# Kernel tuning notes

Measured on AMD Instinct MI355X. Metric: run time of the kernel, lower is better.

The kernel has to match this reference:

```python
import jax, jax.numpy as jnp
import numpy as np

EPS = 1e-8
SEARCH = 21  # search_window_size


def _window_stack(x, S):
    """x: [B,C,Hp,Wp] (already padded). Returns [B,C,H,W,S*S] matching
    torch unfold(2,S,1).unfold(3,S,1).reshape(...,-1) ordering (h-offset major)."""
    B, C, Hp, Wp = x.shape
    H, W = Hp - S + 1, Wp - S + 1
    patches = jax.lax.conv_general_dilated_patches(
        x, filter_shape=(S, S), window_strides=(1, 1), padding='VALID',
        dimension_numbers=('NCHW', 'OIHW', 'NCHW'))  # [B, C*S*S, H, W], (C, u, v) major->minor
    patches = patches.reshape(B, C, S * S, H, W)
    return jnp.transpose(patches, (0, 1, 3, 4, 2))  # [B,C,H,W,S*S]


def setup_inputs() -> dict:
    key = jax.random.key(0)
    k1, k2 = jax.random.split(key)
    rgb = jax.random.uniform(k1, (1, 3, 256, 256), dtype=jnp.float32)  # must be in [0,1]
    h = jnp.array([0.1], dtype=jnp.float32)  # learned NLM bandwidth parameter
    return {"rgb": rgb, "h": h}


def reference(rgb, h):
    S = SEARCH
    pad = (S - 1) // 2
    # luminance (clip only affects y, not the rgb values being averaged)
    rgb_c = jnp.clip(rgb, 0.0, 1.0)
    y = 0.299 * rgb_c[:, :1] + 0.587 * rgb_c[:, 1:2] + 0.114 * rgb_c[:, 2:]  # [B,1,H,W]

    pw = ((0, 0), (0, 0), (pad, pad), (pad, pad))
    rgb_ws = _window_stack(jnp.pad(rgb, pw, mode='reflect'), S)  # [B,3,H,W,S^2]
    y_ws = _window_stack(jnp.pad(y, pw, mode='reflect'), S)      # [B,1,H,W,S^2]

    dis = (y[..., None] - y_ws) ** 2                              # [B,1,H,W,S^2]
    dis_pad = jnp.pad(dis, ((0, 0), (0, 0), (pad, pad), (pad, pad), (0, 0)), mode='reflect')
    # sum of squared diffs over an SxS spatial window per offset (matches unfold+sum)
    dis = jax.lax.reduce_window(dis_pad, 0.0, jax.lax.add,
                                (1, 1, S, S, 1), (1, 1, 1, 1, 1), 'VALID')  # [B,1,H,W,S^2]

    distances = jnp.sqrt(jax.nn.relu(dis))
    weights = jnp.exp(-distances / (jax.nn.relu(h) + EPS))        # [B,1,H,W,S^2]
    denoised = (weights * rgb_ws).sum(-1) / weights.sum(-1)       # [B,3,H,W]
    return jnp.clip(denoised, 0.0, 1.0)
```

## Files before the change

kernel.cpp:

```cpp
#include <hip/hip_runtime.h>
#include <math.h>


#define IMG 256
#define NPIX (IMG * IMG)
#define TILE 32
#define GR 52
#define YD 72
#define YSTR 78
#define HST 54
#define NOFF 441
#define NGB 12

typedef __attribute__((ext_vector_type(4))) _Float16 half4;
typedef __attribute__((ext_vector_type(2))) _Float16 half2_t;

#if __has_builtin(__builtin_amdgcn_fdot2)
#define FDOT2(a, b, c) __builtin_amdgcn_fdot2((a), (b), (c), false)
#else
#define FDOT2(a, b, c) ((c) + (float)(a).x * (float)(b).x + (float)(a).y * (float)(b).y)
#endif

__device__ __forceinline__ int refl(int t) {
    t = t < 0 ? -t : t;
    return t > 255 ? 510 - t : t;
}

template <bool DIRECT>
__global__ __launch_bounds__(256, 3)
void nlm_main(const float* __restrict__ rgb, const float* __restrict__ hptr,
              float4* __restrict__ partials)
{
    __shared__ __align__(16) _Float16 Yreg[YD][YSTR];
    __shared__ __align__(16) _Float16 Creg4[GR][GR][4];
    __shared__ __align__(16) _Float16 hsT[4][TILE][HST];
    __shared__ unsigned char cjTab[21][GR];

    const int tid = threadIdx.x;
    const int tj = ((int)blockIdx.x & 7) * TILE;
    const int ti = ((int)blockIdx.x >> 3) * TILE;

    const int Ybi = min(max(ti - 20, 0), IMG - YD);
    const int Ybj = min(max(tj - 20, 0), IMG - YD);
    const bool interior = (ti >= 20) && (ti + 51 <= 255) && (tj >= 20) && (tj + 51 <= 255);

    for (int idx = tid; idx < YD * YD; idx += 256) {
        int a = idx / YD, b = idx - a * YD;
        int g = (Ybi + a) * IMG + (Ybj + b);
        float r  = fminf(fmaxf(rgb[g], 0.f), 1.f);
        float gg = fminf(fmaxf(rgb[NPIX + g], 0.f), 1.f);
        float bb = fminf(fmaxf(rgb[2 * NPIX + g], 0.f), 1.f);
        Yreg[a][b] = (_Float16)(0.299f * r + 0.587f * gg + 0.114f * bb);
    }
    for (int idx = tid; idx < GR * GR; idx += 256) {
        int t = idx / GR, b = idx - t * GR;
        int g = refl(ti - 10 + t) * IMG + refl(tj - 10 + b);
        half4 c;
        c.x = (_Float16)rgb[g];
        c.y = (_Float16)rgb[NPIX + g];
        c.z = (_Float16)rgb[2 * NPIX + g];
        c.w = (_Float16)0.f;
        *(half4*)&Creg4[t][b][0] = c;
    }
    if (!interior) {
        for (int idx = tid; idx < 21 * GR; idx += 256) {
            int d = idx / GR, c = idx - d * GR;
            cjTab[d][c] = (unsigned char)(refl(refl(tj - 10 + c) + (d - 10)) - Ybj);
        }
    }
    __syncthreads();

    const int lane = tid & 63;
    const int wv   = tid >> 6;
    const bool hact = lane < GR;

    half2_t y0h[26];
    if (hact) {
        if (interior) {
            const half2_t* q0 = (const half2_t*)&Yreg[lane + 10][10];
            #pragma unroll
            for (int i = 0; i < 26; ++i) y0h[i] = q0[i];
        } else {
            const _Float16* Y0row = &Yreg[refl(ti - 10 + lane) - Ybi][0];
            const unsigned char* cj0 = &cjTab[10][0];
            #pragma unroll
            for (int i = 0; i < 26; ++i) {
                half2_t v;
                v.x = Y0row[cj0[2 * i]];
                v.y = Y0row[cj0[2 * i + 1]];
                y0h[i] = v;
            }
        }
    }

    const float hv = fmaxf(hptr[0], 0.f);
    const float negI = -1.0f / (hv + 1e-8f);

    const int pb  = lane & 31;
    const int s16 = (lane >> 5) << 4;

    float aR[16], aG[16], aB[16], aW[16];
    #pragma unroll
    for (int k = 0; k < 16; ++k) { aR[k]=0.f; aG[k]=0.f; aB[k]=0.f; aW[k]=0.f; }

    half2_t one; one.x = (_Float16)1.f; one.y = (_Float16)1.f;

    for (int o = (int)blockIdx.y * 4 + wv; o < NOFF; o += 48) {
        const int oq = o / 21;
        const int du = oq - 10;
        const int dv = o - oq * 21 - 10;

        if (hact) {
            const int t = lane;
            half2_t ff[26];
            if (interior) {
                if ((dv & 1) == 0) {
                    const half2_t* q1 = (const half2_t*)&Yreg[t + 10 + du][10 + dv];
                    #pragma unroll
                    for (int i = 0; i < 26; ++i) {
                        half2_t d2 = y0h[i] - q1[i];
                        ff[i] = d2 * d2;
                    }
                } else {
                    const half2_t* q1 = (const half2_t*)&Yreg[t + 10 + du][10 + dv - 1];
                    half2_t prev = q1[0];
                    #pragma unroll
                    for (int i = 0; i < 26; ++i) {
                        half2_t cur = q1[i + 1];
                        half2_t b; b.x = prev.y; b.y = cur.x;
                        half2_t d2 = y0h[i] - b;
                        ff[i] = d2 * d2;
                        prev = cur;
                    }
                }
            } else {
                const unsigned int* cw = (const unsigned int*)&cjTab[dv + 10][0];
                const _Float16* Y1row = &Yreg[refl(refl(ti - 10 + t) + du) - Ybi][0];
                #pragma unroll
                for (int i = 0; i < 26; ++i) {
                    unsigned int w0 = cw[i >> 1];
                    int sh = (i & 1) * 16;
                    _Float16 a0 = Y1row[(w0 >> sh) & 0xffu];
                    _Float16 a1 = Y1row[(w0 >> (sh + 8)) & 0xffu];
                    half2_t yv; yv.x = a0; yv.y = a1;
                    half2_t d2 = y0h[i] - yv;
                    ff[i] = d2 * d2;
                }
            }
            float s0f = 0.f;
            #pragma unroll
            for (int i = 0; i < 10; ++i) s0f = FDOT2(ff[i], one, s0f);
            s0f += (float)ff[10].x;
            _Float16 s = (_Float16)s0f;
            hsT[wv][0][t] = s;
            #pragma unroll
            for (int k = 1; k < 32; ++k) {
                int ja = 20 + k, jb = k - 1;
                _Float16 fa = (ja & 1) ? ff[ja >> 1].y : ff[ja >> 1].x;
                _Float16 fb = (jb & 1) ? ff[jb >> 1].y : ff[jb >> 1].x;
                s += (_Float16)(fa - fb);
                hsT[wv][k][t] = s;
            }
        }

        {
            const half2_t* col2 = (const half2_t*)&hsT[wv][pb][s16];
            half2_t w2[18];
            #pragma unroll
            for (int i = 0; i < 18; ++i) w2[i] = col2[i];

            float vs = 0.f;
            #pragma unroll
            for (int i = 0; i < 10; ++i) vs = FDOT2(w2[i], one, vs);
            vs += (float)w2[10].x;

            float vss[16];
            vss[0] = vs;
            #pragma unroll
            for (int k = 0; k < 15; ++k) {
                int ja = 21 + k, jb = k;
                _Float16 fa = (ja & 1) ? w2[ja >> 1].y : w2[ja >> 1].x;
                _Float16 fb = (jb & 1) ? w2[jb >> 1].y : w2[jb >> 1].x;
                vss[k + 1] = vss[k] + (float)(_Float16)(fa - fb);
            }

            const int cr = s16 + 10 + du;
            const int cc = pb + 10 + dv;
            #pragma unroll
            for (int k = 0; k < 16; ++k) {
                float dist = sqrtf(fmaxf(vss[k], 0.f));
                float w = __expf(dist * negI);
                half4 c = *(const half4*)&Creg4[cr + k][cc][0];
                aW[k] += w;
                aR[k] += w * (float)c.x;
                aG[k] += w * (float)c.y;
                aB[k] += w * (float)c.z;
            }
        }
    }

    __syncthreads();
    float4* scratch = (float4*)&Creg4[0][0][0];
    #pragma unroll
    for (int w = 0; w < 4; ++w) {
        if (wv == w) {
            #pragma unroll
            for (int k = 0; k < 16; ++k) {
                int px = (s16 + k) * 32 + pb;
                float4 v = make_float4(aR[k], aG[k], aB[k], aW[k]);
                if (w == 0) scratch[px] = v;
                else {
                    float4 a = scratch[px];
                    scratch[px] = make_float4(a.x + v.x, a.y + v.y, a.z + v.z, a.w + v.w);
                }
            }
        }
        __syncthreads();
    }
    for (int i = tid; i < TILE * TILE; i += 256) {
        float4 v = scratch[i];
        int gpix = (ti + (i >> 5)) * IMG + (tj + (i & 31));
        if (DIRECT) {
            partials[(size_t)blockIdx.y * NPIX + gpix] = v;
        } else {
            float* p = (float*)&partials[gpix];
            atomicAdd(p + 0, v.x);
            atomicAdd(p + 1, v.y);
            atomicAdd(p + 2, v.z);
            atomicAdd(p + 3, v.w);
        }
    }
}

template <int NGT>
__global__ __launch_bounds__(256)
void nlm_finalize(const float4* __restrict__ partials, float* __restrict__ out)
{
    int idx = blockIdx.x * blockDim.x + threadIdx.x;
    float r = 0.f, g = 0.f, b = 0.f, w = 0.f;
    #pragma unroll
    for (int gg = 0; gg < NGT; ++gg) {
        float4 p = partials[(size_t)gg * NPIX + idx];
        r += p.x; g += p.y; b += p.z; w += p.w;
    }
    float inv = 1.0f / w;
    out[idx]            = fminf(fmaxf(r * inv, 0.f), 1.f);
    out[NPIX + idx]     = fminf(fmaxf(g * inv, 0.f), 1.f);
    out[2 * NPIX + idx] = fminf(fmaxf(b * inv, 0.f), 1.f);
}

extern "C" void kernel_launch(void* const* d_in, const int* in_sizes, int n_in,
                              void* d_out, int out_size, void* d_ws, size_t ws_size,
                              hipStream_t stream) {
    (void)in_sizes; (void)n_in; (void)out_size;
    const float* rgb  = (const float*)d_in[0];
    const float* hptr = (const float*)d_in[1];
    float* out = (float*)d_out;
    float4* partials = (float4*)d_ws;

    const bool direct = ws_size >= (size_t)NGB * NPIX * sizeof(float4);
    dim3 grid(64, NGB);
    if (direct) {
        nlm_main<true><<<grid, 256, 0, stream>>>(rgb, hptr, partials);
        nlm_finalize<NGB><<<NPIX / 256, 256, 0, stream>>>(partials, out);
    } else {
        (void)hipMemsetAsync(partials, 0, (size_t)NPIX * sizeof(float4), stream);
        nlm_main<false><<<grid, 256, 0, stream>>>(rgb, hptr, partials);
        nlm_finalize<1><<<NPIX / 256, 256, 0, stream>>>(partials, out);
    }
}
```

Measured before the change: 114.2 us.

## Accumulate weighted colors in packed fp16 and split prefix sums into two chains

Replaces the four fp32 per-pixel accumulators with two packed half2 accumulators, storing 1.0 in the color alpha slot so the weight sum comes out of the same packed FMA. It also splits the horizontal and vertical sliding-window running sums into two independent chains to shorten the dependency chains. This reduces register pressure and ALU instructions in the hot loop. In exchange, accumulating up to about 110 weighted terms per pixel in fp16 loses precision, so small weights may round away and accuracy may drift.

```diff
diff --git a/kernel.cpp b/kernel.cpp
--- a/kernel.cpp
+++ b/kernel.cpp
@@ -59,7 +59,7 @@
         c.x = (_Float16)rgb[g];
         c.y = (_Float16)rgb[NPIX + g];
         c.z = (_Float16)rgb[2 * NPIX + g];
-        c.w = (_Float16)0.f;
+        c.w = (_Float16)1.f;
         *(half4*)&Creg4[t][b][0] = c;
     }
     if (!interior) {
@@ -99,9 +99,12 @@
     const int pb  = lane & 31;
     const int s16 = (lane >> 5) << 4;
 
-    float aR[16], aG[16], aB[16], aW[16];
+    half2_t accRG[16], accBW[16];
     #pragma unroll
-    for (int k = 0; k < 16; ++k) { aR[k]=0.f; aG[k]=0.f; aB[k]=0.f; aW[k]=0.f; }
+    for (int k = 0; k < 16; ++k) {
+        accRG[k].x = (_Float16)0.f; accRG[k].y = (_Float16)0.f;
+        accBW[k].x = (_Float16)0.f; accBW[k].y = (_Float16)0.f;
+    }
 
     half2_t one; one.x = (_Float16)1.f; one.y = (_Float16)1.f;
 
@@ -147,19 +150,33 @@
                     ff[i] = d2 * d2;
                 }
             }
-            float s0f = 0.f;
+            float s0f = 0.f, s1f = 0.f;
             #pragma unroll
             for (int i = 0; i < 10; ++i) s0f = FDOT2(ff[i], one, s0f);
             s0f += (float)ff[10].x;
-            _Float16 s = (_Float16)s0f;
-            hsT[wv][0][t] = s;
-            #pragma unroll
-            for (int k = 1; k < 32; ++k) {
-                int ja = 20 + k, jb = k - 1;
-                _Float16 fa = (ja & 1) ? ff[ja >> 1].y : ff[ja >> 1].x;
-                _Float16 fb = (jb & 1) ? ff[jb >> 1].y : ff[jb >> 1].x;
-                s += (_Float16)(fa - fb);
-                hsT[wv][k][t] = s;
+            #pragma unroll
+            for (int i = 8; i < 18; ++i) s1f = FDOT2(ff[i], one, s1f);
+            s1f += (float)ff[18].x;
+            _Float16 sA = (_Float16)s0f;
+            _Float16 sB = (_Float16)s1f;
+            hsT[wv][0][t]  = sA;
+            hsT[wv][16][t] = sB;
+            #pragma unroll
+            for (int k = 1; k < 16; ++k) {
+                {
+                    int ja = 20 + k, jb = k - 1;
+                    _Float16 fa = (ja & 1) ? ff[ja >> 1].y : ff[ja >> 1].x;
+                    _Float16 fb = (jb & 1) ? ff[jb >> 1].y : ff[jb >> 1].x;
+                    sA += (_Float16)(fa - fb);
+                    hsT[wv][k][t] = sA;
+                }
+                {
+                    int ja = 36 + k, jb = 15 + k;
+                    _Float16 fa = (ja & 1) ? ff[ja >> 1].y : ff[ja >> 1].x;
+                    _Float16 fb = (jb & 1) ? ff[jb >> 1].y : ff[jb >> 1].x;
+                    sB += (_Float16)(fa - fb);
+                    hsT[wv][16 + k][t] = sB;
+                }
             }
         }
 
@@ -169,19 +186,31 @@
             #pragma unroll
             for (int i = 0; i < 18; ++i) w2[i] = col2[i];
 
-            float vs = 0.f;
-            #pragma unroll
-            for (int i = 0; i < 10; ++i) vs = FDOT2(w2[i], one, vs);
-            vs += (float)w2[10].x;
+            float vs0 = 0.f, vs1 = 0.f;
+            #pragma unroll
+            for (int i = 0; i < 10; ++i) vs0 = FDOT2(w2[i], one, vs0);
+            vs0 += (float)w2[10].x;
+            #pragma unroll
+            for (int i = 4; i < 14; ++i) vs1 = FDOT2(w2[i], one, vs1);
+            vs1 += (float)w2[14].x;
 
             float vss[16];
-            vss[0] = vs;
-            #pragma unroll
-            for (int k = 0; k < 15; ++k) {
-                int ja = 21 + k, jb = k;
-                _Float16 fa = (ja & 1) ? w2[ja >> 1].y : w2[ja >> 1].x;
-                _Float16 fb = (jb & 1) ? w2[jb >> 1].y : w2[jb >> 1].x;
-                vss[k + 1] = vss[k] + (float)(_Float16)(fa - fb);
+            vss[0] = vs0;
+            vss[8] = vs1;
+            #pragma unroll
+            for (int k = 0; k < 7; ++k) {
+                {
+                    int ja = 21 + k, jb = k;
+                    _Float16 fa = (ja & 1) ? w2[ja >> 1].y : w2[ja >> 1].x;
+                    _Float16 fb = (jb & 1) ? w2[jb >> 1].y : w2[jb >> 1].x;
+                    vss[k + 1] = vss[k] + (float)(_Float16)(fa - fb);
+                }
+                {
+                    int ja = 29 + k, jb = 8 + k;
+                    _Float16 fa = (ja & 1) ? w2[ja >> 1].y : w2[ja >> 1].x;
+                    _Float16 fb = (jb & 1) ? w2[jb >> 1].y : w2[jb >> 1].x;
+                    vss[k + 9] = vss[k + 8] + (float)(_Float16)(fa - fb);
+                }
             }
 
             const int cr = s16 + 10 + du;
@@ -190,11 +219,13 @@
             for (int k = 0; k < 16; ++k) {
                 float dist = sqrtf(fmaxf(vss[k], 0.f));
                 float w = __expf(dist * negI);
-                half4 c = *(const half4*)&Creg4[cr + k][cc][0];
-                aW[k] += w;
-                aR[k] += w * (float)c.x;
-                aG[k] += w * (float)c.y;
-                aB[k] += w * (float)c.z;
+                _Float16 wh = (_Float16)w;
+                half2_t w2v; w2v.x = wh; w2v.y = wh;
+                const half2_t* cp = (const half2_t*)&Creg4[cr + k][cc][0];
+                half2_t cRG = cp[0];
+                half2_t cBW = cp[1];
+                accRG[k] = w2v * cRG + accRG[k];
+                accBW[k] = w2v * cBW + accBW[k];
             }
         }
     }
@@ -207,7 +238,8 @@
             #pragma unroll
             for (int k = 0; k < 16; ++k) {
                 int px = (s16 + k) * 32 + pb;
-                float4 v = make_float4(aR[k], aG[k], aB[k], aW[k]);
+                float4 v = make_float4((float)accRG[k].x, (float)accRG[k].y,
+                                       (float)accBW[k].x, (float)accBW[k].y);
                 if (w == 0) scratch[px] = v;
                 else {
                     float4 a = scratch[px];
```

Result: no change. 112.2 us (-1.8%).
